# Performance work log

Measured on AMD Instinct MI355X. Metric: run time of the kernel, lower is better.

## Reference

```python
import jax, jax.numpy as jnp
import numpy as np

N, D = 8192, 256
ALPHA, BETA, K = 50.0, 1.0, 2


def setup_inputs() -> dict:
    key = jax.random.key(0)
    k1, k2, k3, k4 = jax.random.split(key, 4)
    Q = jax.random.normal(k1, (N, D), dtype=jnp.float32)
    # 0/1 similarity structure; diagonal forced nonzero so no row is fully masked
    sim = jax.random.randint(k2, (N, N), 0, 2).astype(jnp.float32)
    sim = sim.at[jnp.arange(N), jnp.arange(N)].set(1.0)
    # nn.Linear(in_dim, in_dim) params: y = x @ W.T + b
    bound = 1.0 / np.sqrt(D)
    W = jax.random.uniform(k3, (D, D), jnp.float32, -bound, bound)
    b = jax.random.uniform(k4, (D,), jnp.float32, -bound, bound)
    return {"Q": Q, "sim_mat": sim, "W": W, "b": b}


def reference(Q, sim_mat, W, b):
    mask = sim_mat == 0  # (N, N) bool, constant across iterations
    H = Q
    for _ in range(K):
        H_proj = H @ W.T + b                      # (N, d)
        scores = H_proj @ H_proj.T                # (N, N)
        scores = jnp.where(mask, -jnp.inf, scores)
        lamb = jax.nn.softmax(scores, axis=1)     # (N, N)
        numerator = ALPHA * Q + BETA * (lamb @ H)
        denominator = ALPHA + BETA * jnp.sum(lamb, axis=1, keepdims=True)
        H = numerator / denominator
    return H
```

## Files before the change

### kernel.cpp

```cpp
#include <hip/hip_runtime.h>
#include <hip/hip_bf16.h>

#define NN 8192
#define DD 256
#define ALPHA 50.0f
#define BETA 1.0f
#define THR 10.0f
#define KQ 4
#define KEYS (NN / KQ)
#define KTILE 64
#define ITERS (KEYS / KTILE)
#define QROWS 128

typedef __attribute__((ext_vector_type(8))) short short8;
typedef __attribute__((ext_vector_type(4))) float f32x4;

static __device__ __forceinline__ ushort f2bf(float f) {
    union { __hip_bfloat16 h; ushort u; } v;
    v.h = __float2bfloat16(f);
    return v.u;
}
static __device__ __forceinline__ float bf2f(ushort u) {
    union { unsigned u; float f; } v; v.u = ((unsigned)u) << 16;
    return v.f;
}
static __device__ __forceinline__ void gl_lds16(const void* g, void* l) {
    __builtin_amdgcn_global_load_lds(
        (const __attribute__((address_space(1))) unsigned int*)g,
        (__attribute__((address_space(3))) unsigned int*)l, 16, 0, 0);
}

__global__ void k_wconv(const float* __restrict__ W, ushort* __restrict__ Wb) {
    int i = blockIdx.x * 256 + threadIdx.x;
    Wb[i] = f2bf(W[i]);
}

__global__ __launch_bounds__(256) void k_pack(const float* __restrict__ sim,
                                              unsigned* __restrict__ bits) {
    __shared__ unsigned char nibs[256];
    int row = blockIdx.x;
    int tid = threadIdx.x;
    for (int p = 0; p < 8; ++p) {
        int col = p * 1024 + tid * 4;
        float4 v = *reinterpret_cast<const float4*>(sim + (size_t)row * NN + col);
        unsigned char nib = (unsigned char)((v.x != 0.f) | ((v.y != 0.f) << 1) |
                                            ((v.z != 0.f) << 2) | ((v.w != 0.f) << 3));
        nibs[tid] = nib;
        __syncthreads();
        if (tid < 32) {
            unsigned word = 0;
#pragma unroll
            for (int i = 0; i < 8; ++i) word |= ((unsigned)nibs[tid * 8 + i]) << (4 * i);
            bits[row * (NN / 32) + p * 32 + tid] = word;
        }
        __syncthreads();
    }
}

__global__ __launch_bounds__(256) void k_convert(const float* __restrict__ H,
                                                 ushort* __restrict__ Hv,
                                                 ushort* __restrict__ Hvt) {
    __shared__ ushort T[64][72];
    int tile = blockIdx.x;
    int r0 = (tile >> 2) * 64;
    int c0 = (tile & 3) * 64;
    int tid = threadIdx.x;
    int tr = tid >> 4;
    int tc = (tid & 15) * 4;
    for (int i = 0; i < 4; ++i) {
        int r = tr + i * 16;
        float4 v = *reinterpret_cast<const float4*>(H + (size_t)(r0 + r) * DD + c0 + tc);
        ushort4 o;
        o.x = f2bf(v.x); o.y = f2bf(v.y); o.z = f2bf(v.z); o.w = f2bf(v.w);
        *reinterpret_cast<ushort4*>(Hv + (size_t)(r0 + r) * DD + c0 + tc) = o;
        T[tc + 0][r] = o.x; T[tc + 1][r] = o.y; T[tc + 2][r] = o.z; T[tc + 3][r] = o.w;
    }
    __syncthreads();
    for (int i = 0; i < 4; ++i) {
        int c = tr + i * 16;
        ushort4 o;
        o.x = T[c][tc + 0]; o.y = T[c][tc + 1]; o.z = T[c][tc + 2]; o.w = T[c][tc + 3];
        *reinterpret_cast<ushort4*>(Hvt + (size_t)(c0 + c) * NN + r0 + tc) = o;
    }
}

__global__ __launch_bounds__(256) void k_proj(const ushort* __restrict__ Hv,
                                              const ushort* __restrict__ Wb,
                                              const float* __restrict__ b,
                                              ushort* __restrict__ Hp) {
    int w = threadIdx.x >> 6;
    int lane = threadIdx.x & 63;
    int row0 = (blockIdx.x >> 1) * 64 + w * 16;
    int ch = blockIdx.x & 1;
    int lr = lane & 15;
    int lk = lane >> 4;
    short8 af[8];
    for (int kk = 0; kk < 8; ++kk)
        af[kk] = *reinterpret_cast<const short8*>(Hv + (size_t)(row0 + lr) * DD + kk * 32 + lk * 8);
    for (int t = 0; t < 8; ++t) {
        f32x4 acc = {0.f, 0.f, 0.f, 0.f};
        int col = (ch * 8 + t) * 16 + lr;
        for (int kk = 0; kk < 8; ++kk) {
            short8 bf = *reinterpret_cast<const short8*>(Wb + (size_t)col * DD + kk * 32 + lk * 8);
            acc = __builtin_amdgcn_mfma_f32_16x16x32_bf16(af[kk], bf, acc, 0, 0, 0);
        }
        float bias = b[col];
        for (int j = 0; j < 4; ++j) {
            int row = row0 + lk * 4 + j;
            Hp[(size_t)row * DD + col] = f2bf(acc[j] + bias);
        }
    }
}

#define PSTR 40
#define KBYTES (KTILE * 256 * 2)
#define VBYTES (256 * KTILE * 2)
#define PBYTES (8 * 16 * PSTR * 2)
#define SMEM_ATTN (2 * KBYTES + 2 * VBYTES + PBYTES)
__global__ __launch_bounds__(512) void k_attn(const ushort* __restrict__ Hp,
                                              const ushort* __restrict__ Hvt,
                                              const unsigned* __restrict__ bits,
                                              ushort* __restrict__ Opart,
                                              float* __restrict__ mpart,
                                              float* __restrict__ lpart) {
    extern __shared__ char smem[];
    ushort* KlB = (ushort*)smem;
    ushort* VlB = (ushort*)(smem + 2 * KBYTES);
    ushort* Pl  = (ushort*)(smem + 2 * KBYTES + 2 * VBYTES);

    const int tid = threadIdx.x;
    const int w = tid >> 6;
    const int lane = tid & 63;
    const int lr = lane & 15;
    const int lk = lane >> 4;
    const int bid = blockIdx.x;
    const int kq = bid & 3;
    const int qt = bid >> 2;
    const int rw0 = qt * QROWS + w * 16;
    const int kstart = kq * KEYS;

    int kSrc[4], vSrc[4], dstO[4];
#pragma unroll
    for (int i = 0; i < 4; ++i) {
        int S = i * 512 + tid;
        int rK = S >> 5, cpK = S & 31;
        kSrc[i] = rK * 256 + (cpK ^ (rK & 7)) * 8;
        int rV = S >> 3, cpV = S & 7;
        vSrc[i] = rV * NN + (cpV ^ (rV & 7)) * 8;
        dstO[i] = S * 8;
    }
    auto stageK = [&](int buf, int kb) {
        const ushort* Kg = Hp + (size_t)kb * DD;
        ushort* base = KlB + buf * (KTILE * 256);
#pragma unroll
        for (int i = 0; i < 4; ++i) gl_lds16(Kg + kSrc[i], base + dstO[i]);
    };
    auto stageV = [&](int buf, int kb) {
        const ushort* Vg = Hvt + kb;
        ushort* base = VlB + buf * (256 * KTILE);
#pragma unroll
        for (int i = 0; i < 4; ++i) gl_lds16(Vg + vSrc[i], base + dstO[i]);
    };

    int Koff[8];
#pragma unroll
    for (int kk = 0; kk < 8; ++kk)
        Koff[kk] = (lr << 9) + ((((kk << 2) + lk) ^ (lr & 7)) << 4);
    const int vBaseA = (lr << 7) + ((lk ^ (lr & 7)) << 4);
    const int vBaseB = (lr << 7) + (((4 + lk) ^ (lr & 7)) << 4);

    short8 qf[8];
#pragma unroll
    for (int kk = 0; kk < 8; ++kk)
        qf[kk] = *reinterpret_cast<const short8*>(Hp + (size_t)(rw0 + lr) * DD + kk * 32 + lk * 8);

    f32x4 o[17];
#pragma unroll
    for (int t = 0; t < 17; ++t) o[t] = {0.f, 0.f, 0.f, 0.f};
    float m[4] = {-1e30f, -1e30f, -1e30f, -1e30f};

    short8 ones;
#pragma unroll
    for (int e = 0; e < 8; ++e) ones[e] = (short)0x3f80;

    stageK(0, kstart);
    stageV(0, kstart);
    asm volatile("s_waitcnt vmcnt(0)" ::: "memory");
    __builtin_amdgcn_s_barrier();
    __builtin_amdgcn_sched_barrier(0);

    ushort* Pw = Pl + (size_t)w * 16 * PSTR;
    const int rowbase = (rw0 + lk * 4) * (NN / 32);
    int cur = 0;
    for (int it = 0; it < ITERS; ++it) {
        const int kb = kstart + it * KTILE;
        const bool staged = (it + 1 < ITERS);
        if (staged) {
            stageK(cur ^ 1, kb + KTILE);
            stageV(cur ^ 1, kb + KTILE);
        }
        const int wi = kb >> 5;
        unsigned mwa[4], mwb[4];
#pragma unroll
        for (int j = 0; j < 4; ++j) {
            mwa[j] = bits[rowbase + j * (NN / 32) + wi];
            mwb[j] = bits[rowbase + j * (NN / 32) + wi + 1];
        }

        const char* Kb = (const char*)(KlB + cur * (KTILE * 256));
        f32x4 s0a = {0.f,0.f,0.f,0.f}, s1a = {0.f,0.f,0.f,0.f};
        f32x4 s0b = {0.f,0.f,0.f,0.f}, s1b = {0.f,0.f,0.f,0.f};
        __builtin_amdgcn_s_setprio(1);
#pragma unroll
        for (int kk = 0; kk < 8; ++kk) {
            short8 k0a = *reinterpret_cast<const short8*>(Kb + Koff[kk]);
            short8 k1a = *reinterpret_cast<const short8*>(Kb + Koff[kk] + (16 << 9));
            short8 k0b = *reinterpret_cast<const short8*>(Kb + Koff[kk] + (32 << 9));
            short8 k1b = *reinterpret_cast<const short8*>(Kb + Koff[kk] + (48 << 9));
            s0a = __builtin_amdgcn_mfma_f32_16x16x32_bf16(qf[kk], k0a, s0a, 0, 0, 0);
            s1a = __builtin_amdgcn_mfma_f32_16x16x32_bf16(qf[kk], k1a, s1a, 0, 0, 0);
            s0b = __builtin_amdgcn_mfma_f32_16x16x32_bf16(qf[kk], k0b, s0b, 0, 0, 0);
            s1b = __builtin_amdgcn_mfma_f32_16x16x32_bf16(qf[kk], k1b, s1b, 0, 0, 0);
        }
        __builtin_amdgcn_s_setprio(0);

        const char* Vb = (const char*)(VlB + cur * (256 * KTILE));
        {
            float c = -1e30f;
#pragma unroll
            for (int j = 0; j < 4; ++j) {
                float a0 = ((mwa[j] >> lr) & 1u) ? s0a[j] : -1e30f;
                float a1 = ((mwa[j] >> (lr + 16)) & 1u) ? s1a[j] : -1e30f;
                s0a[j] = a0; s1a[j] = a1;
                c = fmaxf(c, fmaxf(a0, a1) - m[j]);
            }
            if (__any(c > THR)) {
#pragma unroll
                for (int j = 0; j < 4; ++j) {
                    float mx = fmaxf(s0a[j], s1a[j]);
                    mx = fmaxf(mx, __shfl_xor(mx, 1));
                    mx = fmaxf(mx, __shfl_xor(mx, 2));
                    mx = fmaxf(mx, __shfl_xor(mx, 4));
                    mx = fmaxf(mx, __shfl_xor(mx, 8));
                    float mn = fmaxf(m[j], mx);
                    float scale = __expf(m[j] - mn);
                    m[j] = mn;
#pragma unroll
                    for (int t = 0; t < 17; ++t) o[t][j] *= scale;
                }
            }
#pragma unroll
            for (int j = 0; j < 4; ++j) {
                Pw[(lk * 4 + j) * PSTR + lr]      = f2bf(__expf(s0a[j] - m[j]));
                Pw[(lk * 4 + j) * PSTR + 16 + lr] = f2bf(__expf(s1a[j] - m[j]));
            }
            asm volatile("s_waitcnt lgkmcnt(0)" ::: "memory");
            __builtin_amdgcn_sched_barrier(0);
            short8 pa = *reinterpret_cast<const short8*>(Pw + lr * PSTR + lk * 8);
            __builtin_amdgcn_s_setprio(1);
#pragma unroll
            for (int t = 0; t < 16; ++t) {
                short8 vf = *reinterpret_cast<const short8*>(Vb + vBaseA + (t << 11));
                o[t] = __builtin_amdgcn_mfma_f32_16x16x32_bf16(pa, vf, o[t], 0, 0, 0);
            }
            o[16] = __builtin_amdgcn_mfma_f32_16x16x32_bf16(pa, ones, o[16], 0, 0, 0);
            __builtin_amdgcn_s_setprio(0);
        }
        {
            float c = -1e30f;
#pragma unroll
            for (int j = 0; j < 4; ++j) {
                float a0 = ((mwb[j] >> lr) & 1u) ? s0b[j] : -1e30f;
                float a1 = ((mwb[j] >> (lr + 16)) & 1u) ? s1b[j] : -1e30f;
                s0b[j] = a0; s1b[j] = a1;
                c = fmaxf(c, fmaxf(a0, a1) - m[j]);
            }
            if (__any(c > THR)) {
#pragma unroll
                for (int j = 0; j < 4; ++j) {
                    float mx = fmaxf(s0b[j], s1b[j]);
                    mx = fmaxf(mx, __shfl_xor(mx, 1));
                    mx = fmaxf(mx, __shfl_xor(mx, 2));
                    mx = fmaxf(mx, __shfl_xor(mx, 4));
                    mx = fmaxf(mx, __shfl_xor(mx, 8));
                    float mn = fmaxf(m[j], mx);
                    float scale = __expf(m[j] - mn);
                    m[j] = mn;
#pragma unroll
                    for (int t = 0; t < 17; ++t) o[t][j] *= scale;
                }
            }
#pragma unroll
            for (int j = 0; j < 4; ++j) {
                Pw[(lk * 4 + j) * PSTR + lr]      = f2bf(__expf(s0b[j] - m[j]));
                Pw[(lk * 4 + j) * PSTR + 16 + lr] = f2bf(__expf(s1b[j] - m[j]));
            }
            asm volatile("s_waitcnt lgkmcnt(0)" ::: "memory");
            __builtin_amdgcn_sched_barrier(0);
            short8 pb = *reinterpret_cast<const short8*>(Pw + lr * PSTR + lk * 8);
            __builtin_amdgcn_s_setprio(1);
#pragma unroll
            for (int t = 0; t < 16; ++t) {
                short8 vf = *reinterpret_cast<const short8*>(Vb + vBaseB + (t << 11));
                o[t] = __builtin_amdgcn_mfma_f32_16x16x32_bf16(pb, vf, o[t], 0, 0, 0);
            }
            o[16] = __builtin_amdgcn_mfma_f32_16x16x32_bf16(pb, ones, o[16], 0, 0, 0);
            __builtin_amdgcn_s_setprio(0);
        }
        if (staged) {
            asm volatile("s_waitcnt vmcnt(0)" ::: "memory");
            __builtin_amdgcn_s_barrier();
            __builtin_amdgcn_sched_barrier(0);
        }
        cur ^= 1;
    }

    ushort* op = Opart + ((size_t)kq * NN + rw0) * DD;
#pragma unroll
    for (int t = 0; t < 16; ++t)
#pragma unroll
        for (int j = 0; j < 4; ++j)
            op[(size_t)(lk * 4 + j) * DD + t * 16 + lr] = f2bf(o[t][j]);
    if (lr == 0) {
#pragma unroll
        for (int j = 0; j < 4; ++j) {
            mpart[kq * NN + rw0 + lk * 4 + j] = m[j];
            lpart[kq * NN + rw0 + lk * 4 + j] = o[16][j];
        }
    }
}

__global__ __launch_bounds__(256) void k_merge4(const ushort* __restrict__ Opart,
                                                const float* __restrict__ mpart,
                                                const float* __restrict__ lpart,
                                                const float* __restrict__ Qo,
                                                float* __restrict__ dst,
                                                ushort* __restrict__ HvOut,
                                                ushort* __restrict__ HvtOut) {
    __shared__ ushort T[32][264];
    int w = threadIdx.x >> 6;
    int lane = threadIdx.x & 63;
    int r0 = blockIdx.x * 32 + w * 8;
    for (int rr = 0; rr < 8; ++rr) {
        int r = r0 + rr;
        float mv[KQ], f[KQ];
        float M = -1e30f;
#pragma unroll
        for (int p = 0; p < KQ; ++p) { mv[p] = mpart[p * NN + r]; M = fmaxf(M, mv[p]); }
        float L = 0.f;
#pragma unroll
        for (int p = 0; p < KQ; ++p) { f[p] = __expf(mv[p] - M); L += f[p] * lpart[p * NN + r]; }
        float invL = 1.0f / L;
        int c = lane * 4;
        float a0 = 0.f, a1 = 0.f, a2 = 0.f, a3 = 0.f;
#pragma unroll
        for (int p = 0; p < KQ; ++p) {
            ushort4 u = *reinterpret_cast<const ushort4*>(Opart + ((size_t)p * NN + r) * DD + c);
            a0 += f[p] * bf2f(u.x); a1 += f[p] * bf2f(u.y);
            a2 += f[p] * bf2f(u.z); a3 += f[p] * bf2f(u.w);
        }
        float4 qv = *reinterpret_cast<const float4*>(Qo + (size_t)r * DD + c);
        float4 ov;
        ov.x = (ALPHA * qv.x + a0 * invL) * (1.0f / (ALPHA + BETA));
        ov.y = (ALPHA * qv.y + a1 * invL) * (1.0f / (ALPHA + BETA));
        ov.z = (ALPHA * qv.z + a2 * invL) * (1.0f / (ALPHA + BETA));
        ov.w = (ALPHA * qv.w + a3 * invL) * (1.0f / (ALPHA + BETA));
        if (dst) *reinterpret_cast<float4*>(dst + (size_t)r * DD + c) = ov;
        ushort4 bv;
        bv.x = f2bf(ov.x); bv.y = f2bf(ov.y); bv.z = f2bf(ov.z); bv.w = f2bf(ov.w);
        if (HvOut) *reinterpret_cast<ushort4*>(HvOut + (size_t)r * DD + c) = bv;
        if (HvtOut) {
            int rl = w * 8 + rr;
            T[rl][c] = bv.x; T[rl][c + 1] = bv.y; T[rl][c + 2] = bv.z; T[rl][c + 3] = bv.w;
        }
    }
    if (HvtOut) {
        __syncthreads();
        int col = threadIdx.x;
        int R0 = blockIdx.x * 32;
        ushort* dstp = HvtOut + (size_t)col * NN + R0;
#pragma unroll
        for (int k = 0; k < 8; ++k) {
            ushort4 u;
            u.x = T[k * 4 + 0][col]; u.y = T[k * 4 + 1][col];
            u.z = T[k * 4 + 2][col]; u.w = T[k * 4 + 3][col];
            *reinterpret_cast<ushort4*>(dstp + k * 4) = u;
        }
    }
}

extern "C" void kernel_launch(void* const* d_in, const int* in_sizes, int n_in,
                              void* d_out, int out_size, void* d_ws, size_t ws_size,
                              hipStream_t stream) {
    const float* Q   = (const float*)d_in[0];
    const float* sim = (const float*)d_in[1];
    const float* W   = (const float*)d_in[2];
    const float* b   = (const float*)d_in[3];
    float* out = (float*)d_out;

    char* ws = (char*)d_ws;
    size_t off = 0;
    ushort* Hv   = (ushort*)(ws + off); off += (size_t)NN * DD * 2;
    ushort* HvtA = (ushort*)(ws + off); off += (size_t)NN * DD * 2;
    ushort* HvtB = (ushort*)(ws + off); off += (size_t)NN * DD * 2;
    ushort* Hp   = (ushort*)(ws + off); off += (size_t)NN * DD * 2;
    ushort* Wb   = (ushort*)(ws + off); off += (size_t)DD * DD * 2;
    unsigned* bits = (unsigned*)(ws + off); off += (size_t)NN * (NN / 32) * 4;
    ushort* Opart = (ushort*)(ws + off); off += (size_t)KQ * NN * DD * 2;
    float*  mpart = (float*)(ws + off);  off += (size_t)KQ * NN * 4;
    float*  lpart = (float*)(ws + off);  off += (size_t)KQ * NN * 4;

    (void)hipFuncSetAttribute((const void*)k_attn,
                              hipFuncAttributeMaxDynamicSharedMemorySize, SMEM_ATTN);

    k_wconv<<<DD * DD / 256, 256, 0, stream>>>(W, Wb);
    k_pack<<<NN, 256, 0, stream>>>(sim, bits);
    k_convert<<<(NN / 64) * (DD / 64), 256, 0, stream>>>(Q, Hv, HvtA);

    k_proj<<<NN / 32, 256, 0, stream>>>(Hv, Wb, b, Hp);
    k_attn<<<(NN / QROWS) * KQ, 512, SMEM_ATTN, stream>>>(Hp, HvtA, bits, Opart, mpart, lpart);
    k_merge4<<<NN / 32, 256, 0, stream>>>(Opart, mpart, lpart, Q, nullptr, Hv, HvtB);

    k_proj<<<NN / 32, 256, 0, stream>>>(Hv, Wb, b, Hp);
    k_attn<<<(NN / QROWS) * KQ, 512, SMEM_ATTN, stream>>>(Hp, HvtB, bits, Opart, mpart, lpart);
    k_merge4<<<NN / 32, 256, 0, stream>>>(Opart, mpart, lpart, Q, out, nullptr, nullptr);
}
```

Before: 298.5 us.

## Transpose QK MFMA and pass softmax probabilities via lane shuffles instead of LDS

Swaps the MFMA operand order so the score tile is laid out transposed: each lane holds scores for one query row across several keys. The running max then becomes a single scalar per lane, reduced with two cross-group shuffles instead of four 16-lane butterfly reductions per row. The bf16 P fragment for the PV MFMA is built directly in registers with __shfl permutes, which removes the per-wave LDS scratch, its s_waitcnt, and the per-row mask loads. The cost is extra shuffle instructions and some select logic, plus broadcasting the rescale factors back to the O accumulator layout.

```diff
diff --git a/kernel.cpp b/kernel.cpp
--- a/kernel.cpp
+++ b/kernel.cpp
@@ -112,11 +112,9 @@
     }
 }
 
-#define PSTR 40
 #define KBYTES (KTILE * 256 * 2)
 #define VBYTES (256 * KTILE * 2)
-#define PBYTES (8 * 16 * PSTR * 2)
-#define SMEM_ATTN (2 * KBYTES + 2 * VBYTES + PBYTES)
+#define SMEM_ATTN (2 * KBYTES + 2 * VBYTES)
 __global__ __launch_bounds__(512) void k_attn(const ushort* __restrict__ Hp,
                                               const ushort* __restrict__ Hvt,
                                               const unsigned* __restrict__ bits,
@@ -126,7 +124,6 @@
     extern __shared__ char smem[];
     ushort* KlB = (ushort*)smem;
     ushort* VlB = (ushort*)(smem + 2 * KBYTES);
-    ushort* Pl  = (ushort*)(smem + 2 * KBYTES + 2 * VBYTES);
 
     const int tid = threadIdx.x;
     const int w = tid >> 6;
@@ -177,7 +174,7 @@
     f32x4 o[17];
 #pragma unroll
     for (int t = 0; t < 17; ++t) o[t] = {0.f, 0.f, 0.f, 0.f};
-    float m[4] = {-1e30f, -1e30f, -1e30f, -1e30f};
+    float m = -1e30f;
 
     short8 ones;
 #pragma unroll
@@ -189,8 +186,10 @@
     __builtin_amdgcn_s_barrier();
     __builtin_amdgcn_sched_barrier(0);
 
-    ushort* Pw = Pl + (size_t)w * 16 * PSTR;
-    const int rowbase = (rw0 + lk * 4) * (NN / 32);
+    const int rowq = (rw0 + lr) * (NN / 32);
+    const int L0 = lr + ((lk & 1) << 5);
+    const int L1 = L0 + 16;
+    const bool lowk = (lk < 2);
     int cur = 0;
     for (int it = 0; it < ITERS; ++it) {
         const int kb = kstart + it * KTILE;
@@ -200,12 +199,6 @@
             stageV(cur ^ 1, kb + KTILE);
         }
         const int wi = kb >> 5;
-        unsigned mwa[4], mwb[4];
-#pragma unroll
-        for (int j = 0; j < 4; ++j) {
-            mwa[j] = bits[rowbase + j * (NN / 32) + wi];
-            mwb[j] = bits[rowbase + j * (NN / 32) + wi + 1];
-        }
 
         const char* Kb = (const char*)(KlB + cur * (KTILE * 256));
         f32x4 s0a = {0.f,0.f,0.f,0.f}, s1a = {0.f,0.f,0.f,0.f};
@@ -217,46 +210,52 @@
             short8 k1a = *reinterpret_cast<const short8*>(Kb + Koff[kk] + (16 << 9));
             short8 k0b = *reinterpret_cast<const short8*>(Kb + Koff[kk] + (32 << 9));
             short8 k1b = *reinterpret_cast<const short8*>(Kb + Koff[kk] + (48 << 9));
-            s0a = __builtin_amdgcn_mfma_f32_16x16x32_bf16(qf[kk], k0a, s0a, 0, 0, 0);
-            s1a = __builtin_amdgcn_mfma_f32_16x16x32_bf16(qf[kk], k1a, s1a, 0, 0, 0);
-            s0b = __builtin_amdgcn_mfma_f32_16x16x32_bf16(qf[kk], k0b, s0b, 0, 0, 0);
-            s1b = __builtin_amdgcn_mfma_f32_16x16x32_bf16(qf[kk], k1b, s1b, 0, 0, 0);
+            s0a = __builtin_amdgcn_mfma_f32_16x16x32_bf16(k0a, qf[kk], s0a, 0, 0, 0);
+            s1a = __builtin_amdgcn_mfma_f32_16x16x32_bf16(k1a, qf[kk], s1a, 0, 0, 0);
+            s0b = __builtin_amdgcn_mfma_f32_16x16x32_bf16(k0b, qf[kk], s0b, 0, 0, 0);
+            s1b = __builtin_amdgcn_mfma_f32_16x16x32_bf16(k1b, qf[kk], s1b, 0, 0, 0);
         }
         __builtin_amdgcn_s_setprio(0);
 
         const char* Vb = (const char*)(VlB + cur * (256 * KTILE));
         {
-            float c = -1e30f;
+            unsigned mw = bits[rowq + wi];
+            float p[8]; float lm = -1e30f;
 #pragma unroll
             for (int j = 0; j < 4; ++j) {
-                float a0 = ((mwa[j] >> lr) & 1u) ? s0a[j] : -1e30f;
-                float a1 = ((mwa[j] >> (lr + 16)) & 1u) ? s1a[j] : -1e30f;
-                s0a[j] = a0; s1a[j] = a1;
-                c = fmaxf(c, fmaxf(a0, a1) - m[j]);
-            }
-            if (__any(c > THR)) {
-#pragma unroll
-                for (int j = 0; j < 4; ++j) {
-                    float mx = fmaxf(s0a[j], s1a[j]);
-                    mx = fmaxf(mx, __shfl_xor(mx, 1));
-                    mx = fmaxf(mx, __shfl_xor(mx, 2));
-                    mx = fmaxf(mx, __shfl_xor(mx, 4));
-                    mx = fmaxf(mx, __shfl_xor(mx, 8));
-                    float mn = fmaxf(m[j], mx);
-                    float scale = __expf(m[j] - mn);
-                    m[j] = mn;
-#pragma unroll
-                    for (int t = 0; t < 17; ++t) o[t][j] *= scale;
-                }
-            }
-#pragma unroll
-            for (int j = 0; j < 4; ++j) {
-                Pw[(lk * 4 + j) * PSTR + lr]      = f2bf(__expf(s0a[j] - m[j]));
-                Pw[(lk * 4 + j) * PSTR + 16 + lr] = f2bf(__expf(s1a[j] - m[j]));
-            }
-            asm volatile("s_waitcnt lgkmcnt(0)" ::: "memory");
-            __builtin_amdgcn_sched_barrier(0);
-            short8 pa = *reinterpret_cast<const short8*>(Pw + lr * PSTR + lk * 8);
+                float a0 = ((mw >> (lk * 4 + j)) & 1u) ? s0a[j] : -1e30f;
+                float a1 = ((mw >> (lk * 4 + j + 16)) & 1u) ? s1a[j] : -1e30f;
+                p[j] = a0; p[4 + j] = a1;
+                lm = fmaxf(lm, fmaxf(a0, a1));
+            }
+            float red = fmaxf(lm, __shfl_xor(lm, 16));
+            red = fmaxf(red, __shfl_xor(red, 32));
+            if (__any(red - m > THR)) {
+                float mn = fmaxf(m, red);
+                float sc = __expf(m - mn);
+                m = mn;
+                float scj[4];
+#pragma unroll
+                for (int j = 0; j < 4; ++j) scj[j] = __shfl(sc, lk * 4 + j);
+#pragma unroll
+                for (int t = 0; t < 17; ++t)
+#pragma unroll
+                    for (int j = 0; j < 4; ++j) o[t][j] *= scj[j];
+            }
+            unsigned b0 = (unsigned)f2bf(__expf(p[0] - m)) | ((unsigned)f2bf(__expf(p[1] - m)) << 16);
+            unsigned b1 = (unsigned)f2bf(__expf(p[2] - m)) | ((unsigned)f2bf(__expf(p[3] - m)) << 16);
+            unsigned b2 = (unsigned)f2bf(__expf(p[4] - m)) | ((unsigned)f2bf(__expf(p[5] - m)) << 16);
+            unsigned b3 = (unsigned)f2bf(__expf(p[6] - m)) | ((unsigned)f2bf(__expf(p[7] - m)) << 16);
+            unsigned lo0 = (unsigned)__shfl((int)b0, L0), lo1 = (unsigned)__shfl((int)b1, L0);
+            unsigned lo2 = (unsigned)__shfl((int)b0, L1), lo3 = (unsigned)__shfl((int)b1, L1);
+            unsigned hi0 = (unsigned)__shfl((int)b2, L0), hi1 = (unsigned)__shfl((int)b3, L0);
+            unsigned hi2 = (unsigned)__shfl((int)b2, L1), hi3 = (unsigned)__shfl((int)b3, L1);
+            union { unsigned u[4]; short8 s; } pau;
+            pau.u[0] = lowk ? lo0 : hi0;
+            pau.u[1] = lowk ? lo1 : hi1;
+            pau.u[2] = lowk ? lo2 : hi2;
+            pau.u[3] = lowk ? lo3 : hi3;
+            short8 pa = pau.s;
             __builtin_amdgcn_s_setprio(1);
 #pragma unroll
             for (int t = 0; t < 16; ++t) {
@@ -267,37 +266,43 @@
             __builtin_amdgcn_s_setprio(0);
         }
         {
-            float c = -1e30f;
+            unsigned mw = bits[rowq + wi + 1];
+            float p[8]; float lm = -1e30f;
 #pragma unroll
             for (int j = 0; j < 4; ++j) {
-                float a0 = ((mwb[j] >> lr) & 1u) ? s0b[j] : -1e30f;
-                float a1 = ((mwb[j] >> (lr + 16)) & 1u) ? s1b[j] : -1e30f;
-                s0b[j] = a0; s1b[j] = a1;
-                c = fmaxf(c, fmaxf(a0, a1) - m[j]);
-            }
-            if (__any(c > THR)) {
-#pragma unroll
-                for (int j = 0; j < 4; ++j) {
-                    float mx = fmaxf(s0b[j], s1b[j]);
-                    mx = fmaxf(mx, __shfl_xor(mx, 1));
-                    mx = fmaxf(mx, __shfl_xor(mx, 2));
-                    mx = fmaxf(mx, __shfl_xor(mx, 4));
-                    mx = fmaxf(mx, __shfl_xor(mx, 8));
-                    float mn = fmaxf(m[j], mx);
-                    float scale = __expf(m[j] - mn);
-                    m[j] = mn;
-#pragma unroll
-                    for (int t = 0; t < 17; ++t) o[t][j] *= scale;
-                }
-            }
-#pragma unroll
-            for (int j = 0; j < 4; ++j) {
-                Pw[(lk * 4 + j) * PSTR + lr]      = f2bf(__expf(s0b[j] - m[j]));
-                Pw[(lk * 4 + j) * PSTR + 16 + lr] = f2bf(__expf(s1b[j] - m[j]));
-            }
-            asm volatile("s_waitcnt lgkmcnt(0)" ::: "memory");
-            __builtin_amdgcn_sched_barrier(0);
-            short8 pb = *reinterpret_cast<const short8*>(Pw + lr * PSTR + lk * 8);
+                float a0 = ((mw >> (lk * 4 + j)) & 1u) ? s0b[j] : -1e30f;
+                float a1 = ((mw >> (lk * 4 + j + 16)) & 1u) ? s1b[j] : -1e30f;
+                p[j] = a0; p[4 + j] = a1;
+                lm = fmaxf(lm, fmaxf(a0, a1));
+            }
+            float red = fmaxf(lm, __shfl_xor(lm, 16));
+            red = fmaxf(red, __shfl_xor(red, 32));
+            if (__any(red - m > THR)) {
+                float mn = fmaxf(m, red);
+                float sc = __expf(m - mn);
+                m = mn;
+                float scj[4];
+#pragma unroll
+                for (int j = 0; j < 4; ++j) scj[j] = __shfl(sc, lk * 4 + j);
+#pragma unroll
+                for (int t = 0; t < 17; ++t)
+#pragma unroll
+                    for (int j = 0; j < 4; ++j) o[t][j] *= scj[j];
+            }
+            unsigned b0 = (unsigned)f2bf(__expf(p[0] - m)) | ((unsigned)f2bf(__expf(p[1] - m)) << 16);
+            unsigned b1 = (unsigned)f2bf(__expf(p[2] - m)) | ((unsigned)f2bf(__expf(p[3] - m)) << 16);
+            unsigned b2 = (unsigned)f2bf(__expf(p[4] - m)) | ((unsigned)f2bf(__expf(p[5] - m)) << 16);
+            unsigned b3 = (unsigned)f2bf(__expf(p[6] - m)) | ((unsigned)f2bf(__expf(p[7] - m)) << 16);
+            unsigned lo0 = (unsigned)__shfl((int)b0, L0), lo1 = (unsigned)__shfl((int)b1, L0);
+            unsigned lo2 = (unsigned)__shfl((int)b0, L1), lo3 = (unsigned)__shfl((int)b1, L1);
+            unsigned hi0 = (unsigned)__shfl((int)b2, L0), hi1 = (unsigned)__shfl((int)b3, L0);
+            unsigned hi2 = (unsigned)__shfl((int)b2, L1), hi3 = (unsigned)__shfl((int)b3, L1);
+            union { unsigned u[4]; short8 s; } pau;
+            pau.u[0] = lowk ? lo0 : hi0;
+            pau.u[1] = lowk ? lo1 : hi1;
+            pau.u[2] = lowk ? lo2 : hi2;
+            pau.u[3] = lowk ? lo3 : hi3;
+            short8 pb = pau.s;
             __builtin_amdgcn_s_setprio(1);
 #pragma unroll
             for (int t = 0; t < 16; ++t) {
@@ -321,12 +326,11 @@
 #pragma unroll
         for (int j = 0; j < 4; ++j)
             op[(size_t)(lk * 4 + j) * DD + t * 16 + lr] = f2bf(o[t][j]);
+    if (lane < 16) mpart[kq * NN + rw0 + lane] = m;
     if (lr == 0) {
 #pragma unroll
-        for (int j = 0; j < 4; ++j) {
-            mpart[kq * NN + rw0 + lk * 4 + j] = m[j];
+        for (int j = 0; j < 4; ++j)
             lpart[kq * NN + rw0 + lk * 4 + j] = o[16][j];
-        }
     }
 }
 
```

Result: slower. 308.6 us (+3.4%).
